# Kernel tuning notes

Hardware: AMD Instinct MI355X
Metric: run time of the kernel (lower is better)

Reference implementation:

```python
import jax, jax.numpy as jnp
import numpy as np

B, C_IN, C_OUT, K, H, W = 8, 512, 512, 3, 32, 32
EPS = 1e-8


def _fir_filter():
    f1 = jnp.array([1.0, 3.0, 3.0, 1.0], dtype=jnp.float32)
    f = jnp.outer(f1, f1)
    f = f / f.sum()
    return f * 4.0  # gain = 2**2, filter.ndim/2 == 1


def setup_inputs() -> dict:
    key = jax.random.key(0)
    k1, k2, k3 = jax.random.split(key, 3)
    x = jax.random.normal(k1, (B, C_IN, H, W), dtype=jnp.float32)
    styles = jax.random.normal(k2, (B, C_IN), dtype=jnp.float32)
    w = jax.random.normal(k3, (C_OUT, C_IN, K, K), dtype=jnp.float32)  # lr_multiplier=1
    return {"x": x, "styles": styles, "w": w}


def reference(x, styles, w):
    batch = x.shape[0]
    gain = 1.0 / np.sqrt(C_OUT * C_IN * K * K)
    # modulate: [B, O, I, kh, kw]
    wm = (w[None] * gain) * (styles[:, None, :, None, None] + 1.0)
    # demodulate
    dcoefs = jax.lax.rsqrt(jnp.sum(wm * wm, axis=(2, 3, 4)) + EPS)  # [B, O]
    wm = wm * dcoefs[:, :, None, None, None]
    # fused modconv: batch folded into channels/groups
    x1 = x.reshape(1, batch * C_IN, H, W)
    # torch conv_transpose2d(stride=2, padding=0, groups=B) == dilated conv with
    # spatially flipped kernel, lhs_dilation=2, padding=K-1 on each side.
    w_eq = jnp.flip(wm, axis=(-2, -1)).reshape(batch * C_OUT, C_IN, K, K)
    y = jax.lax.conv_general_dilated(
        x1, w_eq,
        window_strides=(1, 1),
        padding=[(K - 1, K - 1), (K - 1, K - 1)],
        lhs_dilation=(2, 2),
        feature_group_count=batch,
        dimension_numbers=("NCHW", "OIHW", "NCHW"),
    )  # [1, B*O, 2H+1, 2W+1]
    # Upfirdn2d: up=1, down=1, pad=[1,1,1,1], depthwise 4x4 FIR (cross-correlation;
    # filter is symmetric so no flip needed)
    C = batch * C_OUT
    f = jnp.broadcast_to(_fir_filter()[None, None], (C, 1, 4, 4))
    y = jax.lax.conv_general_dilated(
        y, f,
        window_strides=(1, 1),
        padding=[(1, 1), (1, 1)],
        feature_group_count=C,
        dimension_numbers=("NCHW", "OIHW", "NCHW"),
    )  # [1, B*O, 2H, 2W]
    return y.reshape(batch, C_OUT, 2 * H, 2 * W)
```

## Files before the change

kernel.cpp:

```cpp
#include <hip/hip_runtime.h>
#include <stdint.h>


#define DI __device__ __forceinline__

typedef __bf16 bf16x8 __attribute__((ext_vector_type(8)));
typedef float f32x4 __attribute__((ext_vector_type(4)));

DI float bf2f(ushort u) { union { uint32_t i; float f; } v; v.i = ((uint32_t)u) << 16; return v.f; }
DI ushort f2bf(float f) {
  union { float f; uint32_t i; } v; v.f = f;
  uint32_t x = v.i;
  return (ushort)((x + 0x7FFFu + ((x >> 16) & 1u)) >> 16);
}

#define GAIN (1.0f / 1536.0f)

__global__ __launch_bounds__(256) void k_prep(const float* __restrict__ w,
                                              const float* __restrict__ styles,
                                              const float* __restrict__ x,
                                              ushort* __restrict__ Wm,
                                              ushort* __restrict__ xt) {
  __shared__ union {
    struct { float ss[4096]; float dc[8]; float wred[4][8]; } wp;
    float tl[32][257];
  } sm;
  const int t = threadIdx.x;
  if (blockIdx.x < 512) {
    const int o = blockIdx.x;
#pragma unroll
    for (int j = 0; j < 4; j++) {
      const int idx = (t + j * 256) * 4;
      *(float4*)&sm.wp.ss[idx] = *(const float4*)&styles[idx];
    }
    float wreg[18];
    const float* wp_ = w + o * 4608 + t * 18;
#pragma unroll
    for (int k = 0; k < 9; k++) {
      float2 v2 = *(const float2*)(wp_ + 2 * k);
      wreg[2 * k] = v2.x;
      wreg[2 * k + 1] = v2.y;
    }
    float q0 = 0.f, q1 = 0.f;
#pragma unroll
    for (int k = 0; k < 9; k++) {
      q0 += wreg[k] * wreg[k];
      q1 += wreg[9 + k] * wreg[9 + k];
    }
    __syncthreads();
    float pb[8];
#pragma unroll
    for (int b = 0; b < 8; b++) {
      float s0 = sm.wp.ss[b * 512 + 2 * t] + 1.0f;
      float s1 = sm.wp.ss[b * 512 + 2 * t + 1] + 1.0f;
      pb[b] = s0 * s0 * q0 + s1 * s1 * q1;
    }
#pragma unroll
    for (int b = 0; b < 8; b++)
#pragma unroll
      for (int off = 32; off > 0; off >>= 1) pb[b] += __shfl_down(pb[b], off, 64);
    const int wid = t >> 6, lane = t & 63;
    if (lane == 0) {
#pragma unroll
      for (int b = 0; b < 8; b++) sm.wp.wred[wid][b] = pb[b];
    }
    __syncthreads();
    if (t < 8)
      sm.wp.dc[t] = rsqrtf((sm.wp.wred[0][t] + sm.wp.wred[1][t] + sm.wp.wred[2][t] + sm.wp.wred[3][t]) *
                               (GAIN * GAIN) + 1e-8f);
    __syncthreads();
#pragma unroll
    for (int b = 0; b < 8; b++) {
      const float d = sm.wp.dc[b];
      const float s0 = GAIN * (sm.wp.ss[b * 512 + 2 * t] + 1.0f) * d;
      const float s1 = GAIN * (sm.wp.ss[b * 512 + 2 * t + 1] + 1.0f) * d;
      ushort* base = Wm + ((size_t)(b * 9) * 512 + o) * 512 + 2 * t;
#pragma unroll
      for (int tap = 0; tap < 9; tap++) {
        ushort2 val = make_ushort2(f2bf(wreg[tap] * s0), f2bf(wreg[9 + tap] * s1));
        *(ushort2*)(base + (size_t)tap * 262144) = val;
      }
    }
  } else {
    const int idx = blockIdx.x - 512;
    const int hw0 = (idx & 3) * 256, i0 = ((idx >> 2) & 15) * 32, b = idx >> 6;
    const float* xb = x + b * (512 * 1024);
#pragma unroll
    for (int p = 0; p < 8; p++) {
      const int r = p * 4 + (t >> 6);
      const int c4 = (t & 63) * 4;
      float4 v = *(const float4*)&xb[(i0 + r) * 1024 + hw0 + c4];
      sm.tl[r][c4] = v.x; sm.tl[r][c4 + 1] = v.y; sm.tl[r][c4 + 2] = v.z; sm.tl[r][c4 + 3] = v.w;
    }
    __syncthreads();
    ushort* xtb = xt + b * (1024 * 512);
#pragma unroll
    for (int p = 0; p < 8; p++) {
      const int hw = p * 32 + (t >> 3);
      const int i4 = (t & 7) * 4;
      ushort4 v = make_ushort4(f2bf(sm.tl[i4][hw]), f2bf(sm.tl[i4 + 1][hw]),
                               f2bf(sm.tl[i4 + 2][hw]), f2bf(sm.tl[i4 + 3][hw]));
      *(ushort4*)&xtb[(hw0 + hw) * 512 + i0 + i4] = v;
    }
  }
}

__global__ __launch_bounds__(512, 2) void k_gemm(const ushort* __restrict__ A,
                                                 const ushort* __restrict__ Bt,
                                                 ushort* __restrict__ C) {
  __shared__ __attribute__((aligned(128))) char smem[131072];
  const int id = blockIdx.x;
  const int batch = id & 7;
  const int rem = id >> 3;
  const int tap = rem >> 3;
  const int t8 = rem & 7;
  const int mt = t8 >> 2, nt = t8 & 3;
  const int m0 = mt * 256, n0 = nt * 256;
  const ushort* Ag = A + (size_t)(batch * 9 + tap) * (512 * 512);
  const ushort* Bg = Bt + (size_t)batch * (1024 * 512);
  ushort* Cg = C + (size_t)(batch * 9 + tap) * (512 * 1024);

  const int tid = threadIdx.x;
  const int w = tid >> 6, lane = tid & 63;
  const int wm = w >> 2, wn = w & 3;
  const int lq = lane >> 4, l15 = lane & 15, l7 = lane & 7;
  const int rlow = lane >> 3;
  const int ssw = (lane & 7) ^ rlow;

  const char* pA = (const char*)Ag + (size_t)(m0 + w * 8 + rlow) * 1024 + ssw * 16;
  const char* pB = (const char*)Bg + (size_t)(n0 + w * 8 + rlow) * 1024 + ssw * 16;
  char* sAd = smem + w * 1024;
  char* sBd = smem + 32768 + w * 1024;

#define GLL(srcp, dstp)                                                                     \
  __builtin_amdgcn_global_load_lds((const __attribute__((address_space(1))) void*)(srcp),   \
                                   (__attribute__((address_space(3))) void*)(dstp), 16, 0, 0)
#define STAGE_A(buf, h, kt)                                                                 \
  do {                                                                                      \
    GLL(pA + (h) * 131072 + (kt) * 128,         sAd + (buf) * 65536 + (h) * 16384);         \
    GLL(pA + (h) * 131072 + 65536 + (kt) * 128, sAd + (buf) * 65536 + (h) * 16384 + 8192);  \
  } while (0)
#define STAGE_B(buf, h, kt)                                                                 \
  do {                                                                                      \
    GLL(pB + (h) * 131072 + (kt) * 128,         sBd + (buf) * 65536 + (h) * 16384);         \
    GLL(pB + (h) * 131072 + 65536 + (kt) * 128, sBd + (buf) * 65536 + (h) * 16384 + 8192);  \
  } while (0)
#define CF asm volatile("" ::: "memory")
#define BAR()                          \
  do {                                 \
    CF;                                \
    __builtin_amdgcn_s_barrier();      \
    CF;                                \
  } while (0)

  const char* Ard = smem + wm * 16384 + l15 * 128;
  const char* Brd = smem + 32768 + (wn >> 1) * 16384 + (wn & 1) * 8192 + l15 * 128;
  const int s0o = (lq ^ l7) * 16;
  const int s1o = ((4 + lq) ^ l7) * 16;

  f32x4 acc[8][4];
  const f32x4 z4 = {0.f, 0.f, 0.f, 0.f};
#pragma unroll
  for (int i = 0; i < 8; ++i)
#pragma unroll
    for (int n = 0; n < 4; ++n) acc[i][n] = z4;

  STAGE_A(0, 0, 0); STAGE_A(0, 1, 0); STAGE_B(0, 0, 0); STAGE_B(0, 1, 0);
  STAGE_A(1, 0, 1); STAGE_A(1, 1, 1); STAGE_B(1, 0, 1); STAGE_B(1, 1, 1);
  asm volatile("s_waitcnt vmcnt(8)" ::: "memory");
  BAR();

#pragma unroll
  for (int t = 0; t < 8; ++t) {
    const int buf = t & 1;
    const char* Ab = Ard + buf * 65536;
    const char* Bb = Brd + buf * 65536;
    bf16x8 a[4][2], b[4][2];
#pragma unroll
    for (int i = 0; i < 4; ++i) {
      a[i][0] = *(const bf16x8*)(Ab + i * 2048 + s0o);
      a[i][1] = *(const bf16x8*)(Ab + i * 2048 + s1o);
    }
#pragma unroll
    for (int n = 0; n < 2; ++n) {
      b[n][0] = *(const bf16x8*)(Bb + n * 2048 + s0o);
      b[n][1] = *(const bf16x8*)(Bb + n * 2048 + s1o);
    }
    BAR();
    __builtin_amdgcn_s_setprio(1);
#pragma unroll
    for (int n = 0; n < 2; ++n)
#pragma unroll
      for (int i = 0; i < 4; ++i) {
        acc[i][n] = __builtin_amdgcn_mfma_f32_16x16x32_bf16(a[i][0], b[n][0], acc[i][n], 0, 0, 0);
        acc[i][n] = __builtin_amdgcn_mfma_f32_16x16x32_bf16(a[i][1], b[n][1], acc[i][n], 0, 0, 0);
      }
    __builtin_amdgcn_s_setprio(0);
    BAR();
#pragma unroll
    for (int n = 2; n < 4; ++n) {
      b[n][0] = *(const bf16x8*)(Bb + n * 2048 + s0o);
      b[n][1] = *(const bf16x8*)(Bb + n * 2048 + s1o);
    }
    BAR();
    __builtin_amdgcn_s_setprio(1);
#pragma unroll
    for (int n = 2; n < 4; ++n)
#pragma unroll
      for (int i = 0; i < 4; ++i) {
        acc[i][n] = __builtin_amdgcn_mfma_f32_16x16x32_bf16(a[i][0], b[n][0], acc[i][n], 0, 0, 0);
        acc[i][n] = __builtin_amdgcn_mfma_f32_16x16x32_bf16(a[i][1], b[n][1], acc[i][n], 0, 0, 0);
      }
    __builtin_amdgcn_s_setprio(0);
    BAR();
    bf16x8 a2[4][2];
#pragma unroll
    for (int i = 0; i < 4; ++i) {
      a2[i][0] = *(const bf16x8*)(Ab + (4 + i) * 2048 + s0o);
      a2[i][1] = *(const bf16x8*)(Ab + (4 + i) * 2048 + s1o);
    }
    if (t < 6) { STAGE_B(buf, 0, t + 2); STAGE_B(buf, 1, t + 2); }
    BAR();
    __builtin_amdgcn_s_setprio(1);
#pragma unroll
    for (int n = 0; n < 2; ++n)
#pragma unroll
      for (int i = 0; i < 4; ++i) {
        acc[4 + i][n] = __builtin_amdgcn_mfma_f32_16x16x32_bf16(a2[i][0], b[n][0], acc[4 + i][n], 0, 0, 0);
        acc[4 + i][n] = __builtin_amdgcn_mfma_f32_16x16x32_bf16(a2[i][1], b[n][1], acc[4 + i][n], 0, 0, 0);
      }
    __builtin_amdgcn_s_setprio(0);
    BAR();
    if (t < 6) { STAGE_A(buf, 0, t + 2); STAGE_A(buf, 1, t + 2); }
    BAR();
    __builtin_amdgcn_s_setprio(1);
#pragma unroll
    for (int n = 2; n < 4; ++n)
#pragma unroll
      for (int i = 0; i < 4; ++i) {
        acc[4 + i][n] = __builtin_amdgcn_mfma_f32_16x16x32_bf16(a2[i][0], b[n][0], acc[4 + i][n], 0, 0, 0);
        acc[4 + i][n] = __builtin_amdgcn_mfma_f32_16x16x32_bf16(a2[i][1], b[n][1], acc[4 + i][n], 0, 0, 0);
      }
    __builtin_amdgcn_s_setprio(0);
    if (t < 6) {
      asm volatile("s_waitcnt vmcnt(8)" ::: "memory");
    } else if (t == 6) {
      asm volatile("s_waitcnt vmcnt(0)" ::: "memory");
    }
    BAR();
  }

  ushort* cs = (ushort*)smem;
#pragma unroll
  for (int p = 0; p < 2; ++p) {
    if (p) BAR();
    if (wm == p) {
#pragma unroll
      for (int mi2 = 0; mi2 < 8; ++mi2)
#pragma unroll
        for (int n = 0; n < 4; ++n) {
          const int row = mi2 * 16 + lq * 4;
          const int col = wn * 64 + n * 16 + l15;
          const f32x4 v = acc[mi2][n];
#pragma unroll
          for (int r = 0; r < 4; ++r) cs[(row + r) * 264 + col] = f2bf(v[r]);
        }
    }
    BAR();
#pragma unroll
    for (int j = 0; j < 8; ++j) {
      const int idx = j * 512 + tid;
      const int row = idx >> 5, c = idx & 31;
      *(uint4*)(Cg + (size_t)(m0 + p * 128 + row) * 1024 + n0 + c * 8) =
          *(const uint4*)(cs + row * 264 + c * 8);
    }
  }
#undef GLL
#undef STAGE_A
#undef STAGE_B
#undef CF
#undef BAR
}

__global__ __launch_bounds__(512) void k_fir(const ushort* __restrict__ C,
                                             float* __restrict__ out) {
  const int bo = blockIdx.x;
  const int b = bo >> 9, o = bo & 511;
  __shared__ __attribute__((aligned(16))) ushort Ct[9 * 1024];
  __shared__ float V[3 * 64 * 36];
  const ushort* Cb = C + ((size_t)(b * 9) * 512 + o) * 1024;
  for (int c = threadIdx.x; c < 1152; c += 512) {
    const int tap = c >> 7, off = (c & 127) * 8;
    *(uint4*)&Ct[tap * 1024 + off] = *(const uint4*)&Cb[(size_t)tap * 524288 + off];
  }
  __syncthreads();
#pragma unroll
  for (int j = 0; j < 3; j++) {
    const int gidx = threadIdx.x + j * 512;
    const int kw = gidx >> 9;
    const int rem = gidx & 511;
    const int u = rem >> 3;
    const int w0 = (rem & 7) * 4;
    float a0 = 0.f, a1 = 0.f, a2 = 0.f, a3 = 0.f;
#pragma unroll
    for (int kh = 0; kh < 3; kh++) {
      const int s0 = (kh + 1 + u) & 1;
#pragma unroll
      for (int d = 0; d < 2; d++) {
        const int h = (u + s0 + 2 * d - 1 - kh) >> 1;
        const bool ok = (h >= 0) & (h < 32);
        const float cf = ok ? ((s0 == d) ? 1.f : 3.f) : 0.f;
        const int hh = ok ? h : 0;
        const uint2 cv = *(const uint2*)&Ct[kh * 3072 + kw * 1024 + hh * 32 + w0];
        a0 += cf * bf2f((ushort)(cv.x & 0xffff));
        a1 += cf * bf2f((ushort)(cv.x >> 16));
        a2 += cf * bf2f((ushort)(cv.y & 0xffff));
        a3 += cf * bf2f((ushort)(cv.y >> 16));
      }
    }
    *(float4*)&V[kw * 2304 + u * 36 + w0] = make_float4(a0, a1, a2, a3);
  }
  __syncthreads();
  const size_t ob = (size_t)bo * 4096;
#pragma unroll
  for (int j = 0; j < 2; j++) {
    const int px4 = threadIdx.x + j * 512;
    const int u = px4 >> 4;
    const int v0 = (px4 & 15) * 4;
    float r[4] = {0.f, 0.f, 0.f, 0.f};
#pragma unroll
    for (int q = 0; q < 4; q++) {
      const int v = v0 + q;
#pragma unroll
      for (int kw = 0; kw < 3; kw++) {
        const int t0 = (kw + 1 + v) & 1;
#pragma unroll
        for (int d = 0; d < 2; d++) {
          const int wx = (v + t0 + 2 * d - 1 - kw) >> 1;
          const bool ok = (wx >= 0) & (wx < 32);
          const float cf = ok ? ((t0 == d) ? 1.f : 3.f) : 0.f;
          const int ww = ok ? wx : 0;
          r[q] += cf * V[kw * 2304 + u * 36 + ww];
        }
      }
      r[q] *= 0.0625f;
    }
    *(float4*)&out[ob + u * 64 + v0] = make_float4(r[0], r[1], r[2], r[3]);
  }
}

extern "C" void kernel_launch(void* const* d_in, const int* in_sizes, int n_in,
                              void* d_out, int out_size, void* d_ws, size_t ws_size,
                              hipStream_t stream) {
  (void)in_sizes; (void)n_in; (void)out_size; (void)ws_size;
  const float* x = (const float*)d_in[0];
  const float* styles = (const float*)d_in[1];
  const float* w = (const float*)d_in[2];
  float* out = (float*)d_out;
  char* ws = (char*)d_ws;
  ushort* Wm = (ushort*)ws;
  ushort* XT = (ushort*)(ws + 37748736);
  ushort* C = (ushort*)(ws + 37748736 + 8388608);

  k_prep<<<1024, 256, 0, stream>>>(w, styles, x, Wm, XT);
  k_gemm<<<576, 512, 0, stream>>>(Wm, XT, C);
  k_fir<<<4096, 512, 0, stream>>>(C, out);
}
```

Before: 165.6 us.

## Retile GEMM to 192x256 tiles over merged tap dimension, shrink LDS

The per-batch GEMM now treats all 9 taps as one M=4608 dimension and tiles it with 192x256 blocks instead of 256x256 per tap, launching 768 blocks instead of 576. This reduces the LDS footprint to 112 KiB and the accumulator registers per thread, aiming at better occupancy and finer load balance across CUs. It also drops one barrier before the last MFMA group and retunes the vmcnt waits to match the new load counts. The trade-off is lower arithmetic intensity per tile and a different staging schedule that could expose memory latency.

```diff
diff --git a/kernel.cpp b/kernel.cpp
--- a/kernel.cpp
+++ b/kernel.cpp
@@ -108,17 +108,15 @@
 __global__ __launch_bounds__(512, 2) void k_gemm(const ushort* __restrict__ A,
                                                  const ushort* __restrict__ Bt,
                                                  ushort* __restrict__ C) {
-  __shared__ __attribute__((aligned(128))) char smem[131072];
+  __shared__ __attribute__((aligned(128))) char smem[114688];
   const int id = blockIdx.x;
   const int batch = id & 7;
   const int rem = id >> 3;
-  const int tap = rem >> 3;
-  const int t8 = rem & 7;
-  const int mt = t8 >> 2, nt = t8 & 3;
-  const int m0 = mt * 256, n0 = nt * 256;
-  const ushort* Ag = A + (size_t)(batch * 9 + tap) * (512 * 512);
+  const int mt = rem >> 2, nt = rem & 3;
+  const int m0 = mt * 192, n0 = nt * 256;
+  const ushort* Ag = A + (size_t)batch * (4608 * 512);
   const ushort* Bg = Bt + (size_t)batch * (1024 * 512);
-  ushort* Cg = C + (size_t)(batch * 9 + tap) * (512 * 1024);
+  ushort* Cg = C + (size_t)batch * (4608 * 1024);
 
   const int tid = threadIdx.x;
   const int w = tid >> 6, lane = tid & 63;
@@ -127,23 +125,26 @@
   const int rlow = lane >> 3;
   const int ssw = (lane & 7) ^ rlow;
 
-  const char* pA = (const char*)Ag + (size_t)(m0 + w * 8 + rlow) * 1024 + ssw * 16;
-  const char* pB = (const char*)Bg + (size_t)(n0 + w * 8 + rlow) * 1024 + ssw * 16;
-  char* sAd = smem + w * 1024;
-  char* sBd = smem + 32768 + w * 1024;
+  const char* pA = (const char*)Ag + (size_t)(m0 + w * 24 + rlow) * 1024 + ssw * 16;
+  const char* pB = (const char*)Bg + (size_t)(n0 + w * 32 + rlow) * 1024 + ssw * 16;
+  char* dA = smem + w * 3072;
+  char* dB = smem + 49152 + w * 4096;
 
 #define GLL(srcp, dstp)                                                                     \
   __builtin_amdgcn_global_load_lds((const __attribute__((address_space(1))) void*)(srcp),   \
                                    (__attribute__((address_space(3))) void*)(dstp), 16, 0, 0)
-#define STAGE_A(buf, h, kt)                                                                 \
-  do {                                                                                      \
-    GLL(pA + (h) * 131072 + (kt) * 128,         sAd + (buf) * 65536 + (h) * 16384);         \
-    GLL(pA + (h) * 131072 + 65536 + (kt) * 128, sAd + (buf) * 65536 + (h) * 16384 + 8192);  \
+#define STAGE_A(buf, kt)                                            \
+  do {                                                              \
+    GLL(pA + 0 * 8192 + (kt) * 128, dA + (buf) * 24576 + 0 * 1024); \
+    GLL(pA + 1 * 8192 + (kt) * 128, dA + (buf) * 24576 + 1 * 1024); \
+    GLL(pA + 2 * 8192 + (kt) * 128, dA + (buf) * 24576 + 2 * 1024); \
   } while (0)
-#define STAGE_B(buf, h, kt)                                                                 \
-  do {                                                                                      \
-    GLL(pB + (h) * 131072 + (kt) * 128,         sBd + (buf) * 65536 + (h) * 16384);         \
-    GLL(pB + (h) * 131072 + 65536 + (kt) * 128, sBd + (buf) * 65536 + (h) * 16384 + 8192);  \
+#define STAGE_B(buf, kt)                                            \
+  do {                                                              \
+    GLL(pB + 0 * 8192 + (kt) * 128, dB + (buf) * 32768 + 0 * 1024); \
+    GLL(pB + 1 * 8192 + (kt) * 128, dB + (buf) * 32768 + 1 * 1024); \
+    GLL(pB + 2 * 8192 + (kt) * 128, dB + (buf) * 32768 + 2 * 1024); \
+    GLL(pB + 3 * 8192 + (kt) * 128, dB + (buf) * 32768 + 3 * 1024); \
   } while (0)
 #define CF asm volatile("" ::: "memory")
 #define BAR()                          \
@@ -153,31 +154,31 @@
     CF;                                \
   } while (0)
 
-  const char* Ard = smem + wm * 16384 + l15 * 128;
-  const char* Brd = smem + 32768 + (wn >> 1) * 16384 + (wn & 1) * 8192 + l15 * 128;
+  const char* Ard = smem + (wm * 96 + l15) * 128;
+  const char* Brd = smem + 49152 + (wn * 64 + l15) * 128;
   const int s0o = (lq ^ l7) * 16;
   const int s1o = ((4 + lq) ^ l7) * 16;
 
-  f32x4 acc[8][4];
+  f32x4 acc[6][4];
   const f32x4 z4 = {0.f, 0.f, 0.f, 0.f};
 #pragma unroll
-  for (int i = 0; i < 8; ++i)
+  for (int i = 0; i < 6; ++i)
 #pragma unroll
     for (int n = 0; n < 4; ++n) acc[i][n] = z4;
 
-  STAGE_A(0, 0, 0); STAGE_A(0, 1, 0); STAGE_B(0, 0, 0); STAGE_B(0, 1, 0);
-  STAGE_A(1, 0, 1); STAGE_A(1, 1, 1); STAGE_B(1, 0, 1); STAGE_B(1, 1, 1);
-  asm volatile("s_waitcnt vmcnt(8)" ::: "memory");
+  STAGE_A(0, 0); STAGE_B(0, 0);
+  STAGE_A(1, 1); STAGE_B(1, 1);
+  asm volatile("s_waitcnt vmcnt(7)" ::: "memory");
   BAR();
 
 #pragma unroll
   for (int t = 0; t < 8; ++t) {
     const int buf = t & 1;
-    const char* Ab = Ard + buf * 65536;
-    const char* Bb = Brd + buf * 65536;
-    bf16x8 a[4][2], b[4][2];
-#pragma unroll
-    for (int i = 0; i < 4; ++i) {
+    const char* Ab = Ard + buf * 24576;
+    const char* Bb = Brd + buf * 32768;
+    bf16x8 a[3][2], a2[3][2], b[4][2];
+#pragma unroll
+    for (int i = 0; i < 3; ++i) {
       a[i][0] = *(const bf16x8*)(Ab + i * 2048 + s0o);
       a[i][1] = *(const bf16x8*)(Ab + i * 2048 + s1o);
     }
@@ -189,12 +190,12 @@
     BAR();
     __builtin_amdgcn_s_setprio(1);
 #pragma unroll
-    for (int n = 0; n < 2; ++n)
-#pragma unroll
-      for (int i = 0; i < 4; ++i) {
-        acc[i][n] = __builtin_amdgcn_mfma_f32_16x16x32_bf16(a[i][0], b[n][0], acc[i][n], 0, 0, 0);
-        acc[i][n] = __builtin_amdgcn_mfma_f32_16x16x32_bf16(a[i][1], b[n][1], acc[i][n], 0, 0, 0);
-      }
+    for (int kk = 0; kk < 2; ++kk)
+#pragma unroll
+      for (int n = 0; n < 2; ++n)
+#pragma unroll
+        for (int i = 0; i < 3; ++i)
+          acc[i][n] = __builtin_amdgcn_mfma_f32_16x16x32_bf16(a[i][kk], b[n][kk], acc[i][n], 0, 0, 0);
     __builtin_amdgcn_s_setprio(0);
     BAR();
 #pragma unroll
@@ -205,45 +206,43 @@
     BAR();
     __builtin_amdgcn_s_setprio(1);
 #pragma unroll
-    for (int n = 2; n < 4; ++n)
-#pragma unroll
-      for (int i = 0; i < 4; ++i) {
-        acc[i][n] = __builtin_amdgcn_mfma_f32_16x16x32_bf16(a[i][0], b[n][0], acc[i][n], 0, 0, 0);
-        acc[i][n] = __builtin_amdgcn_mfma_f32_16x16x32_bf16(a[i][1], b[n][1], acc[i][n], 0, 0, 0);
-      }
+    for (int kk = 0; kk < 2; ++kk)
+#pragma unroll
+      for (int n = 2; n < 4; ++n)
+#pragma unroll
+        for (int i = 0; i < 3; ++i)
+          acc[i][n] = __builtin_amdgcn_mfma_f32_16x16x32_bf16(a[i][kk], b[n][kk], acc[i][n], 0, 0, 0);
     __builtin_amdgcn_s_setprio(0);
     BAR();
-    bf16x8 a2[4][2];
-#pragma unroll
-    for (int i = 0; i < 4; ++i) {
-      a2[i][0] = *(const bf16x8*)(Ab + (4 + i) * 2048 + s0o);
-      a2[i][1] = *(const bf16x8*)(Ab + (4 + i) * 2048 + s1o);
-    }
-    if (t < 6) { STAGE_B(buf, 0, t + 2); STAGE_B(buf, 1, t + 2); }
+#pragma unroll
+    for (int i = 0; i < 3; ++i) {
+      a2[i][0] = *(const bf16x8*)(Ab + (3 + i) * 2048 + s0o);
+      a2[i][1] = *(const bf16x8*)(Ab + (3 + i) * 2048 + s1o);
+    }
+    if (t < 6) STAGE_B(buf, t + 2);
     BAR();
     __builtin_amdgcn_s_setprio(1);
 #pragma unroll
-    for (int n = 0; n < 2; ++n)
-#pragma unroll
-      for (int i = 0; i < 4; ++i) {
-        acc[4 + i][n] = __builtin_amdgcn_mfma_f32_16x16x32_bf16(a2[i][0], b[n][0], acc[4 + i][n], 0, 0, 0);
-        acc[4 + i][n] = __builtin_amdgcn_mfma_f32_16x16x32_bf16(a2[i][1], b[n][1], acc[4 + i][n], 0, 0, 0);
-      }
+    for (int kk = 0; kk < 2; ++kk)
+#pragma unroll
+      for (int n = 0; n < 2; ++n)
+#pragma unroll
+        for (int i = 0; i < 3; ++i)
+          acc[3 + i][n] = __builtin_amdgcn_mfma_f32_16x16x32_bf16(a2[i][kk], b[n][kk], acc[3 + i][n], 0, 0, 0);
     __builtin_amdgcn_s_setprio(0);
     BAR();
-    if (t < 6) { STAGE_A(buf, 0, t + 2); STAGE_A(buf, 1, t + 2); }
-    BAR();
+    if (t < 6) STAGE_A(buf, t + 2);
     __builtin_amdgcn_s_setprio(1);
 #pragma unroll
-    for (int n = 2; n < 4; ++n)
-#pragma unroll
-      for (int i = 0; i < 4; ++i) {
-        acc[4 + i][n] = __builtin_amdgcn_mfma_f32_16x16x32_bf16(a2[i][0], b[n][0], acc[4 + i][n], 0, 0, 0);
-        acc[4 + i][n] = __builtin_amdgcn_mfma_f32_16x16x32_bf16(a2[i][1], b[n][1], acc[4 + i][n], 0, 0, 0);
-      }
+    for (int kk = 0; kk < 2; ++kk)
+#pragma unroll
+      for (int n = 2; n < 4; ++n)
+#pragma unroll
+        for (int i = 0; i < 3; ++i)
+          acc[3 + i][n] = __builtin_amdgcn_mfma_f32_16x16x32_bf16(a2[i][kk], b[n][kk], acc[3 + i][n], 0, 0, 0);
     __builtin_amdgcn_s_setprio(0);
     if (t < 6) {
-      asm volatile("s_waitcnt vmcnt(8)" ::: "memory");
+      asm volatile("s_waitcnt vmcnt(7)" ::: "memory");
     } else if (t == 6) {
       asm volatile("s_waitcnt vmcnt(0)" ::: "memory");
     }
@@ -256,22 +255,22 @@
     if (p) BAR();
     if (wm == p) {
 #pragma unroll
-      for (int mi2 = 0; mi2 < 8; ++mi2)
+      for (int mi = 0; mi < 6; ++mi)
 #pragma unroll
         for (int n = 0; n < 4; ++n) {
-          const int row = mi2 * 16 + lq * 4;
+          const int row = mi * 16 + lq * 4;
           const int col = wn * 64 + n * 16 + l15;
-          const f32x4 v = acc[mi2][n];
+          const f32x4 v = acc[mi][n];
 #pragma unroll
           for (int r = 0; r < 4; ++r) cs[(row + r) * 264 + col] = f2bf(v[r]);
         }
     }
     BAR();
 #pragma unroll
-    for (int j = 0; j < 8; ++j) {
+    for (int j = 0; j < 6; ++j) {
       const int idx = j * 512 + tid;
       const int row = idx >> 5, c = idx & 31;
-      *(uint4*)(Cg + (size_t)(m0 + p * 128 + row) * 1024 + n0 + c * 8) =
+      *(uint4*)(Cg + (size_t)(m0 + p * 96 + row) * 1024 + n0 + c * 8) =
           *(const uint4*)(cs + row * 264 + c * 8);
     }
   }
@@ -363,6 +362,6 @@
   ushort* C = (ushort*)(ws + 37748736 + 8388608);
 
   k_prep<<<1024, 256, 0, stream>>>(w, styles, x, Wm, XT);
-  k_gemm<<<576, 512, 0, stream>>>(Wm, XT, C);
+  k_gemm<<<768, 512, 0, stream>>>(Wm, XT, C);
   k_fir<<<4096, 512, 0, stream>>>(C, out);
 }
```

After: 157.0 us. 5.2% less time.
